# Optimization experiments

Hardware: AMD Instinct MI355X
Metric: run time of the kernel (lower is better)

The kernel has to match this reference:

```python
import jax, jax.numpy as jnp
import numpy as np

THRESH = 1e-5   # replace_denormals threshold
EPS = 1e-5      # instance_norm eps

NUM_LAYERS, TOKEN_LEN, EMBED = 24, 100, 1024
N, B = 1025, 8  # seq (incl. cls token), batch


def _replace_denormals(x):
    return jnp.where((x < THRESH) & (x > -THRESH), THRESH, x)


def _delta_feat(feats, tokens, w_t2f, b_t2f, w_df, b_df, instance_norm):
    # feats: [n, b, c], tokens: [m, c]
    attn = jnp.einsum('nbc,mc->nbm', feats, tokens)
    if instance_norm:  # normalize over m per (n, b), biased variance (torch F.instance_norm)
        mu = attn.mean(axis=-1, keepdims=True)
        var = attn.var(axis=-1, keepdims=True)
        attn = (attn - mu) / jnp.sqrt(var + EPS)
    attn = jax.nn.softmax(attn * (feats.shape[-1] ** -0.5), axis=-1)
    v = tokens[1:] @ w_t2f.T + b_t2f                     # [m-1, c]
    df = jnp.einsum('nbm,mc->nbc', attn[:, :, 1:], v)    # drop first token column
    return (df + feats) @ w_df.T + b_df


def setup_inputs() -> dict:
    key = jax.random.key(0)
    ks = jax.random.split(key, 12)
    C = EMBED
    inp = {
        'feats': jax.random.normal(ks[0], (N, B, C), dtype=jnp.float32),
        'learnable_tokens': jax.random.normal(ks[1], (NUM_LAYERS, TOKEN_LEN, C), dtype=jnp.float32) * 0.04,
        'learnable_tokens2': jax.random.normal(ks[2], (NUM_LAYERS, TOKEN_LEN, C), dtype=jnp.float32) * 0.04,
        'w_t2f': jax.random.normal(ks[3], (C, C), dtype=jnp.float32) * 0.02,
        'b_t2f': jax.random.normal(ks[4], (C,), dtype=jnp.float32) * 0.02,
        'w_df': jax.random.normal(ks[5], (C, C), dtype=jnp.float32) * 0.02,
        'b_df': jax.random.normal(ks[6], (C,), dtype=jnp.float32) * 0.02,
        'w_t2f2': jax.random.normal(ks[7], (C, C), dtype=jnp.float32) * 0.02,
        'b_t2f2': jax.random.normal(ks[8], (C,), dtype=jnp.float32) * 0.02,
        'w_df2': jax.random.normal(ks[9], (C, C), dtype=jnp.float32) * 0.02,
        'b_df2': jax.random.normal(ks[10], (C,), dtype=jnp.float32) * 0.02,
        'scale': jnp.float32(0.001),
        'layer': 0,
    }
    return inp


def reference(feats, learnable_tokens, learnable_tokens2,
              w_t2f, b_t2f, w_df, b_df,
              w_t2f2, b_t2f2, w_df2, b_df2,
              scale, layer):
    # batch_first=False, has_cls_token=True (defaults)
    C = feats.shape[-1]
    cls_tok, x = feats[:1], feats[1:]            # [1,b,c], [n,b,c]
    n, b = x.shape[0], x.shape[1]

    # decompose: fft2 over last two dims (b, c), norm='backward'
    f = jnp.fft.fft2(x)
    re, im = jnp.real(f), jnp.imag(f)
    amp = jnp.sqrt(_replace_denormals(re * re + im * im))
    phase = jnp.arctan2(im, _replace_denormals(re))

    t1 = learnable_tokens[layer]
    t2 = learnable_tokens2[layer]
    d_phase = _delta_feat(phase, t1, w_t2f, b_t2f, w_df, b_df, instance_norm=False)
    d_amp = _delta_feat(amp, t2, w_t2f2, b_t2f2, w_df2, b_df2, instance_norm=True)

    # compose: stacked last dim has size 2, dim 2 has size C -> divide by sqrt(C*2)
    z = (jnp.cos(d_phase) * d_amp + 1j * (jnp.sin(d_phase) * d_amp)) / np.float32(np.sqrt(C * 2.0))
    z = z[..., : C // 2 + 1]                      # torch irfft2 trims last dim to s[-1]//2+1
    delta = jnp.fft.irfft2(z, s=(b, C), norm='ortho')

    out = x + delta * scale
    return jnp.concatenate([cls_tok, out], axis=0)
```

## Files before the change

kernel.cpp:

```cpp
#include <hip/hip_runtime.h>
#include <cstddef>


using bf16x8 = __attribute__((ext_vector_type(8))) short;
using f32x4  = __attribute__((ext_vector_type(4))) float;

__device__ inline short f2bf(float f) {
  union { float f; unsigned u; } v; v.f = f;
  unsigned r = v.u + 0x7FFFu + ((v.u >> 16) & 1u);
  return (short)(r >> 16);
}
__device__ inline float bf2f(short s) {
  union { unsigned u; float f; } v; v.u = ((unsigned)(unsigned short)s) << 16;
  return v.f;
}
__device__ inline void async16(const void* g, void* l) {
  __builtin_amdgcn_global_load_lds(
      (const __attribute__((address_space(1))) void*)g,
      (__attribute__((address_space(3))) void*)l, 16, 0, 0);
}
__device__ inline float fast_atan2(float y, float x) {
  float ax = fabsf(x), ay = fabsf(y);
  float mx = fmaxf(ax, ay), mn = fminf(ax, ay);
  float a = mn * __frcp_rn(mx);
  float s = a * a;
  float r = fmaf(fmaf(fmaf(-0.0464964749f, s, 0.15931422f), s, -0.327622764f),
                 s * a, a);
  if (ay > ax) r = 1.5707963267948966f - r;
  if (x < 0.f) r = 3.14159265358979f - r;
  return (y < 0.f) ? -r : r;
}

__device__ inline int PADi(int i) { return i + (i >> 5); }
__device__ inline int rev4_8(int t) {
  return ((t & 3) << 6) | (((t >> 2) & 3) << 4) | (((t >> 4) & 3) << 2) | ((t >> 6) & 3);
}

__device__ inline void fft8_fwd(float* xr, float* xi) {
  const float r = 0.70710678118654752f;
  float ar[4], ai[4], br[4], bi[4], tr, ti;
  ar[0]=xr[0]+xr[4]; ai[0]=xi[0]+xi[4]; br[0]=xr[0]-xr[4]; bi[0]=xi[0]-xi[4];
  ar[1]=xr[1]+xr[5]; ai[1]=xi[1]+xi[5];
  tr=xr[1]-xr[5]; ti=xi[1]-xi[5]; br[1]=(tr+ti)*r; bi[1]=(ti-tr)*r;
  ar[2]=xr[2]+xr[6]; ai[2]=xi[2]+xi[6];
  tr=xr[2]-xr[6]; ti=xi[2]-xi[6]; br[2]=ti; bi[2]=-tr;
  ar[3]=xr[3]+xr[7]; ai[3]=xi[3]+xi[7];
  tr=xr[3]-xr[7]; ti=xi[3]-xi[7]; br[3]=(ti-tr)*r; bi[3]=-(tr+ti)*r;
  float u0r=ar[0]+ar[2], u0i=ai[0]+ai[2], u1r=ar[1]+ar[3], u1i=ai[1]+ai[3];
  float v0r=ar[0]-ar[2], v0i=ai[0]-ai[2];
  tr=ar[1]-ar[3]; ti=ai[1]-ai[3];
  float v1r=ti, v1i=-tr;
  xr[0]=u0r+u1r; xi[0]=u0i+u1i; xr[4]=u0r-u1r; xi[4]=u0i-u1i;
  xr[2]=v0r+v1r; xi[2]=v0i+v1i; xr[6]=v0r-v1r; xi[6]=v0i-v1i;
  u0r=br[0]+br[2]; u0i=bi[0]+bi[2]; u1r=br[1]+br[3]; u1i=bi[1]+bi[3];
  v0r=br[0]-br[2]; v0i=bi[0]-bi[2];
  tr=br[1]-br[3]; ti=bi[1]-bi[3];
  v1r=ti; v1i=-tr;
  xr[1]=u0r+u1r; xi[1]=u0i+u1i; xr[5]=u0r-u1r; xi[5]=u0i-u1i;
  xr[3]=v0r+v1r; xi[3]=v0i+v1i; xr[7]=v0r-v1r; xi[7]=v0i-v1i;
}
__device__ inline void fft8_inv(float* xr, float* xi) {
  const float r = 0.70710678118654752f;
  float ar[4], ai[4], br[4], bi[4], tr, ti;
  ar[0]=xr[0]+xr[4]; ai[0]=xi[0]+xi[4]; br[0]=xr[0]-xr[4]; bi[0]=xi[0]-xi[4];
  ar[1]=xr[1]+xr[5]; ai[1]=xi[1]+xi[5];
  tr=xr[1]-xr[5]; ti=xi[1]-xi[5]; br[1]=(tr-ti)*r; bi[1]=(tr+ti)*r;
  ar[2]=xr[2]+xr[6]; ai[2]=xi[2]+xi[6];
  tr=xr[2]-xr[6]; ti=xi[2]-xi[6]; br[2]=-ti; bi[2]=tr;
  ar[3]=xr[3]+xr[7]; ai[3]=xi[3]+xi[7];
  tr=xr[3]-xr[7]; ti=xi[3]-xi[7]; br[3]=-(tr+ti)*r; bi[3]=(tr-ti)*r;
  float u0r=ar[0]+ar[2], u0i=ai[0]+ai[2], u1r=ar[1]+ar[3], u1i=ai[1]+ai[3];
  float v0r=ar[0]-ar[2], v0i=ai[0]-ai[2];
  tr=ar[1]-ar[3]; ti=ai[1]-ai[3];
  float v1r=-ti, v1i=tr;
  xr[0]=u0r+u1r; xi[0]=u0i+u1i; xr[4]=u0r-u1r; xi[4]=u0i-u1i;
  xr[2]=v0r+v1r; xi[2]=v0i+v1i; xr[6]=v0r-v1r; xi[6]=v0i-v1i;
  u0r=br[0]+br[2]; u0i=bi[0]+bi[2]; u1r=br[1]+br[3]; u1i=bi[1]+bi[3];
  v0r=br[0]-br[2]; v0i=bi[0]-bi[2];
  tr=br[1]-br[3]; ti=bi[1]-bi[3];
  v1r=-ti; v1i=tr;
  xr[1]=u0r+u1r; xi[1]=u0i+u1i; xr[5]=u0r-u1r; xi[5]=u0i-u1i;
  xr[3]=v0r+v1r; xi[3]=v0i+v1i; xr[7]=v0r-v1r; xi[7]=v0i-v1i;
}

template <int SIGN, int NP>
__device__ inline void fft1024xN(float2 (*zb)[1056], int t) {
#pragma unroll
  for (int s = 0; s < 5; ++s) {
    const int Q = 256 >> (2 * s);
    const int j = t & (Q - 1);
    const int i0 = ((t & ~(Q - 1)) << 2) + j;
    const float ang = (float)SIGN * 6.283185307179586f * (float)j / (float)(4 * Q);
    float s1, c1; __sincosf(ang, &s1, &c1);
    const float c2 = c1 * c1 - s1 * s1, s2 = 2.f * c1 * s1;
    const float c3 = c2 * c1 - s2 * s1, s3 = c2 * s1 + s2 * c1;
#pragma unroll
    for (int p = 0; p < NP; ++p) {
      float2* z = zb[p];
      float2 x0 = z[PADi(i0)];
      float2 x1 = z[PADi(i0 + Q)];
      float2 x2 = z[PADi(i0 + 2 * Q)];
      float2 x3 = z[PADi(i0 + 3 * Q)];
      float t0x = x0.x + x2.x, t0y = x0.y + x2.y;
      float t1x = x0.x - x2.x, t1y = x0.y - x2.y;
      float t2x = x1.x + x3.x, t2y = x1.y + x3.y;
      float t3x = x1.x - x3.x, t3y = x1.y - x3.y;
      float u0x = t0x + t2x, u0y = t0y + t2y;
      float u2x = t0x - t2x, u2y = t0y - t2y;
      float u1x, u1y, u3x, u3y;
      if (SIGN < 0) { u1x = t1x + t3y; u1y = t1y - t3x; u3x = t1x - t3y; u3y = t1y + t3x; }
      else          { u1x = t1x - t3y; u1y = t1y + t3x; u3x = t1x + t3y; u3y = t1y - t3x; }
      z[PADi(i0)]         = make_float2(u0x, u0y);
      z[PADi(i0 + Q)]     = make_float2(u1x * c1 - u1y * s1, u1x * s1 + u1y * c1);
      z[PADi(i0 + 2 * Q)] = make_float2(u2x * c2 - u2y * s2, u2x * s2 + u2y * c2);
      z[PADi(i0 + 3 * Q)] = make_float2(u3x * c3 - u3y * s3, u3x * s3 + u3y * c3);
    }
    __syncthreads();
  }
}

__global__ __launch_bounds__(256) void fwd_fft2_amp_conv(
    const float* __restrict__ feats,
    short* __restrict__ ampb, short* __restrict__ phaseb,
    const float* __restrict__ w1, const float* __restrict__ w2,
    const float* __restrict__ w3, const float* __restrict__ w4,
    const float* __restrict__ lt1, const float* __restrict__ lt2,
    const int* __restrict__ layerp,
    short* __restrict__ Wdst, short* __restrict__ Tdst,
    float* __restrict__ out) {
  if (blockIdx.x >= 1024) {
    const int id = blockIdx.x - 1024;
    const int t4 = threadIdx.x * 4;
    if (id < 4096) {
      const int z = id >> 10, row = id & 1023;
      const float* W = (z == 0 ? w1 : z == 1 ? w2 : z == 2 ? w3 : w4)
                       + (size_t)row * 1024;
      short* D = Wdst + ((size_t)z * 1024 + row) * 1024;
      float4 v = *(const float4*)(W + t4);
      D[t4] = f2bf(v.x); D[t4 + 1] = f2bf(v.y); D[t4 + 2] = f2bf(v.z); D[t4 + 3] = f2bf(v.w);
    } else if (id < 4608) {
      const int i2 = id - 4096;
      const int zz = i2 >> 7, row = i2 & 127;
      const int z = zz & 1, shift = zz >> 1;
      short* D = Tdst + ((size_t)zz * 128 + row) * 1024;
      if (row + shift < 100) {
        const float* S = (z ? lt2 : lt1) + (size_t)layerp[0] * 102400
                         + (size_t)(row + shift) * 1024;
        float4 v = *(const float4*)(S + t4);
        D[t4] = f2bf(v.x); D[t4 + 1] = f2bf(v.y); D[t4 + 2] = f2bf(v.z); D[t4 + 3] = f2bf(v.w);
      } else {
        D[t4] = 0; D[t4 + 1] = 0; D[t4 + 2] = 0; D[t4 + 3] = 0;
      }
    } else {
      const int i = (id - 4608) * 256 + threadIdx.x;
      out[i] = feats[i];
    }
    return;
  }
  __shared__ float2 zb[4][1056];
  const int t = threadIdx.x;
  const int n = blockIdx.x;
  const float* base = feats + 8192 + (size_t)n * 8192;
#pragma unroll
  for (int p = 0; p < 4; ++p) {
    const float* x0 = base + (size_t)(2 * p) * 1024;
    const float* x1 = x0 + 1024;
#pragma unroll
    for (int m = 0; m < 4; ++m) {
      const int c = t + 256 * m;
      zb[p][PADi(c)] = make_float2(x0[c], x1[c]);
    }
  }
  __syncthreads();
  fft1024xN<-1, 4>(zb, t);
  const int rt = rev4_8(t);
  short* ab = ampb + (size_t)n * 8192;
  short* pb = phaseb + (size_t)n * 8192;
#pragma unroll
  for (int m = 0; m < 4; ++m) {
    const int k = 256 * m + t;
    const int kk = (1024 - k) & 1023;
    const int pos  = 4 * rt + m;
    const int pos2 = 4 * rev4_8(kk & 255) + (kk >> 8);
    float xr[8], xi[8];
#pragma unroll
    for (int p = 0; p < 4; ++p) {
      float2 Z = zb[p][PADi(pos)];
      float2 W = zb[p][PADi(pos2)];
      xr[2 * p]     = 0.5f * (Z.x + W.x);
      xi[2 * p]     = 0.5f * (Z.y - W.y);
      xr[2 * p + 1] = 0.5f * (Z.y + W.y);
      xi[2 * p + 1] = 0.5f * (W.x - Z.x);
    }
    fft8_fwd(xr, xi);
#pragma unroll
    for (int kb = 0; kb < 8; ++kb) {
      float sr = xr[kb], si = xi[kb];
      float r2 = sr * sr + si * si;
      if (r2 < 1e-5f) r2 = 1e-5f;
      float a = sqrtf(r2);
      float rr = (sr < 1e-5f && sr > -1e-5f) ? 1e-5f : sr;
      float ph = fast_atan2(si, rr);
      ab[kb * 1024 + k] = f2bf(a);
      pb[kb * 1024 + k] = f2bf(ph);
    }
  }
}

__global__ __launch_bounds__(256) void gemm_sm_v(
    const short* A0, const short* A1,
    const short* Tok,
    const short* Wall,
    const float* bt1, const float* bt2,
    short* __restrict__ awb,
    short* __restrict__ vrow) {
  __shared__ __align__(16) char smem[39040];
  const int z = blockIdx.z;
  const int tid = threadIdx.x;
  const int wave = tid >> 6, lane = tid & 63;
  const int m16 = lane & 15, quad = lane >> 4;
  const int fcol = ((quad ^ ((m16 >> 1) & 3)) * 8) + m16 * 32;
  const int r0 = tid >> 2;
  const int csw = (((tid & 3) ^ ((r0 >> 1) & 3)) * 8);

  if (blockIdx.x >= 256) {
    const int jb = blockIdx.x - 256;
    const short* A = Tok + (size_t)(2 + z) * 128 * 1024;
    const short* B = Wall + (size_t)z * 1024 * 1024;
    const float* bias = z ? bt2 : bt1;
    short* C = vrow + (size_t)z * 128 * 1024;
    const int K = 1024;
    short* As = (short*)smem;
    short* Bs = (short*)(smem + 8192);
    const int wm = (wave & 1) * 64, wn = (wave >> 1) * 64;
    f32x4 acc[4][4];
#pragma unroll
    for (int i = 0; i < 4; ++i)
#pragma unroll
      for (int j = 0; j < 4; ++j) acc[i][j] = (f32x4){0.f, 0.f, 0.f, 0.f};
    const short* aSrc0 = A + (size_t)r0 * K + csw;
    const short* aSrc1 = aSrc0 + (size_t)64 * K;
    const short* bSrc0 = B + (size_t)(jb * 128 + r0) * K + csw;
    const short* bSrc1 = bSrc0 + (size_t)64 * K;
    short* aDst0 = As + tid * 8;
    short* aDst1 = As + 2048 + tid * 8;
    short* bDst0 = Bs + tid * 8;
    short* bDst1 = Bs + 2048 + tid * 8;
    for (int k0 = 0; k0 < K; k0 += 32) {
      async16(aSrc0 + k0, aDst0);
      async16(aSrc1 + k0, aDst1);
      async16(bSrc0 + k0, bDst0);
      async16(bSrc1 + k0, bDst1);
      __syncthreads();
      bf16x8 af[4], bg[4];
#pragma unroll
      for (int ib = 0; ib < 4; ++ib)
        af[ib] = *(const bf16x8*)(As + (wm + ib * 16) * 32 + fcol);
#pragma unroll
      for (int jb2 = 0; jb2 < 4; ++jb2)
        bg[jb2] = *(const bf16x8*)(Bs + (wn + jb2 * 16) * 32 + fcol);
#pragma unroll
      for (int ib = 0; ib < 4; ++ib)
#pragma unroll
        for (int jb2 = 0; jb2 < 4; ++jb2)
          acc[ib][jb2] = __builtin_amdgcn_mfma_f32_16x16x32_bf16(af[ib], bg[jb2], acc[ib][jb2], 0, 0, 0);
      __syncthreads();
    }
#pragma unroll
    for (int ib = 0; ib < 4; ++ib) {
      const int rowb = wm + ib * 16 + quad * 4;
#pragma unroll
      for (int jb2 = 0; jb2 < 4; ++jb2) {
        const int col = jb * 128 + wn + jb2 * 16 + m16;
        const float bcv = bias[col];
#pragma unroll
        for (int r = 0; r < 4; ++r)
          C[(size_t)(rowb + r) * 1024 + col] = f2bf(acc[ib][jb2][r] + bcv);
      }
    }
    return;
  }

  const short* A = z ? A1 : A0;
  const short* B = Tok + (size_t)z * 128 * 1024;
  const int K = 1024;
  short* As = (short*)smem;
  short* Bs = (short*)(smem + 4096);
  float (*ltile)[129] = (float(*)[129])(smem + 20480);
  float (*red1)[8] = (float(*)[8])(smem + 36992);
  float (*red2)[8] = (float(*)[8])(smem + 38016);
  const int wm = (wave & 1) * 16, wn = (wave >> 1) * 64;
  f32x4 acc[4];
#pragma unroll
  for (int j = 0; j < 4; ++j) acc[j] = (f32x4){0.f, 0.f, 0.f, 0.f};
  const int asub = tid >> 7, aidx = tid & 127;
  const int ar0 = aidx >> 2;
  const int acsw = (((aidx & 3) ^ ((ar0 >> 1) & 3)) * 8);
  const short* aSrc = A + (size_t)(blockIdx.x * 32 + ar0) * K + acsw + asub * 32;
  short* aDst = As + asub * 1024 + aidx * 8;
  const short* bSrc0 = B + (size_t)r0 * K + csw;
  const short* bSrc1 = bSrc0 + (size_t)64 * K;
  short* bDst00 = Bs + tid * 8;
  short* bDst01 = Bs + 2048 + tid * 8;
  short* bDst10 = Bs + 4096 + tid * 8;
  short* bDst11 = Bs + 4096 + 2048 + tid * 8;
  for (int k0 = 0; k0 < K; k0 += 64) {
    async16(aSrc + k0, aDst);
    async16(bSrc0 + k0, bDst00);
    async16(bSrc1 + k0, bDst01);
    async16(bSrc0 + k0 + 32, bDst10);
    async16(bSrc1 + k0 + 32, bDst11);
    __syncthreads();
#pragma unroll
    for (int sub = 0; sub < 2; ++sub) {
      bf16x8 af = *(const bf16x8*)(As + sub * 1024 + wm * 32 + fcol);
      bf16x8 bg[4];
#pragma unroll
      for (int jb = 0; jb < 4; ++jb)
        bg[jb] = *(const bf16x8*)(Bs + sub * 4096 + (wn + jb * 16) * 32 + fcol);
#pragma unroll
      for (int jb = 0; jb < 4; ++jb)
        acc[jb] = __builtin_amdgcn_mfma_f32_16x16x32_bf16(af, bg[jb], acc[jb], 0, 0, 0);
    }
    __syncthreads();
  }
#pragma unroll
  for (int jb = 0; jb < 4; ++jb)
#pragma unroll
    for (int r = 0; r < 4; ++r)
      ltile[wm + quad * 4 + r][wn + jb * 16 + m16] = acc[jb][r];
  __syncthreads();
  const int row = tid >> 3, l8 = tid & 7;
  float s = 0.f, q = 0.f;
  for (int c = l8; c < 100; c += 8) { float x = ltile[row][c]; s += x; q += x * x; }
  red1[row][l8] = s; red2[row][l8] = q;
  __syncthreads();
  float ssum = 0.f, qsum = 0.f;
#pragma unroll
  for (int i = 0; i < 8; ++i) { ssum += red1[row][i]; qsum += red2[row][i]; }
  __syncthreads();
  const float mu = ssum * 0.01f;
  const float rinv = rsqrtf(fmaxf(qsum * 0.01f - mu * mu, 0.f) + 1e-5f);
  float mx = -3.4e38f;
  for (int c = l8; c < 100; c += 8) {
    float x = ltile[row][c];
    if (z == 1) x = (x - mu) * rinv;
    x *= 0.03125f;
    ltile[row][c] = x;
    mx = fmaxf(mx, x);
  }
  red1[row][l8] = mx;
  __syncthreads();
#pragma unroll
  for (int i = 0; i < 8; ++i) mx = fmaxf(mx, red1[row][i]);
  __syncthreads();
  float es = 0.f;
  for (int c = l8; c < 100; c += 8) {
    float e = __expf(ltile[row][c] - mx);
    ltile[row][c] = e; es += e;
  }
  red1[row][l8] = es;
  __syncthreads();
  float tot = 0.f;
#pragma unroll
  for (int i = 0; i < 8; ++i) tot += red1[row][i];
  const float inv = 1.f / tot;
  short* Aout = awb + ((size_t)z * 8192 + (size_t)blockIdx.x * 32 + row) * 128;
  for (int c = l8; c < 100; c += 8)
    if (c >= 1) Aout[c - 1] = f2bf(ltile[row][c] * inv);
  for (int k = l8; k < 128; k += 8)
    if (k >= 99) Aout[k] = 0;
}

__global__ __launch_bounds__(256) void gemm64(
    const short* A0, const short* A1,
    const short* B0, const short* B1,
    void* C0v, void* C1v, int K, int ldc) {
  const int z = blockIdx.z;
  const short* A = z ? A1 : A0;
  const short* B = z ? B1 : B0;
  void* Cv = z ? C1v : C0v;
  __shared__ __align__(16) short As[64 * 32];
  __shared__ __align__(16) short Bs[128 * 32];
  const int tid = threadIdx.x;
  const int wave = tid >> 6, lane = tid & 63;
  const int m16 = lane & 15, quad = lane >> 4;
  const int wm = (wave & 1) * 32, wn = (wave >> 1) * 64;
  f32x4 acc[2][4];
#pragma unroll
  for (int i = 0; i < 2; ++i)
#pragma unroll
    for (int j = 0; j < 4; ++j) acc[i][j] = (f32x4){0.f, 0.f, 0.f, 0.f};
  const int r0 = tid >> 2;
  const int csw = (((tid & 3) ^ ((r0 >> 1) & 3)) * 8);
  const short* aSrc  = A + (size_t)(blockIdx.x * 64 + r0) * K + csw;
  const short* bSrc0 = B + (size_t)r0 * K + csw;
  const short* bSrc1 = bSrc0 + (size_t)64 * K;
  short* aDst  = As + tid * 8;
  short* bDst0 = Bs + tid * 8;
  short* bDst1 = Bs + 2048 + tid * 8;
  const int fcol = ((quad ^ ((m16 >> 1) & 3)) * 8) + m16 * 32;
  for (int k0 = 0; k0 < K; k0 += 32) {
    async16(aSrc + k0, aDst);
    async16(bSrc0 + k0, bDst0);
    async16(bSrc1 + k0, bDst1);
    __syncthreads();
    bf16x8 af[2], bg[4];
#pragma unroll
    for (int ib = 0; ib < 2; ++ib)
      af[ib] = *(const bf16x8*)(As + (wm + ib * 16) * 32 + fcol);
#pragma unroll
    for (int jb = 0; jb < 4; ++jb)
      bg[jb] = *(const bf16x8*)(Bs + (wn + jb * 16) * 32 + fcol);
#pragma unroll
    for (int ib = 0; ib < 2; ++ib)
#pragma unroll
      for (int jb = 0; jb < 4; ++jb)
        acc[ib][jb] = __builtin_amdgcn_mfma_f32_16x16x32_bf16(af[ib], bg[jb], acc[ib][jb], 0, 0, 0);
    __syncthreads();
  }
#pragma unroll
  for (int ib = 0; ib < 2; ++ib) {
    const int rowb = blockIdx.x * 64 + wm + ib * 16 + quad * 4;
#pragma unroll
    for (int jb = 0; jb < 4; ++jb) {
      const int col = wn + jb * 16 + m16;
#pragma unroll
      for (int r = 0; r < 4; ++r)
        ((short*)Cv)[(size_t)(rowb + r) * ldc + col] = f2bf(acc[ib][jb][r]);
    }
  }
}

__global__ __launch_bounds__(256) void gemm128_dual(
    const short* A1_0, const short* A1_1,
    const short* B1_0, const short* B1_1,
    const short* A2_0, const short* A2_1,
    const short* B2_0, const short* B2_1,
    const float* bias0, const float* bias1,
    short* C0, short* C1, int K1, int K2, int ldc) {
  const int z = blockIdx.z;
  const short* A1 = z ? A1_1 : A1_0;
  const short* B1 = z ? B1_1 : B1_0;
  const short* A2 = z ? A2_1 : A2_0;
  const short* B2 = z ? B2_1 : B2_0;
  const float* bias = z ? bias1 : bias0;
  short* C = z ? C1 : C0;
  __shared__ __align__(16) short As[2][128 * 32];
  __shared__ __align__(16) short Bs[2][128 * 32];
  const int tid = threadIdx.x;
  const int wave = tid >> 6, lane = tid & 63;
  const int m16 = lane & 15, quad = lane >> 4;
  const int wm = (wave & 1) * 64, wn = (wave >> 1) * 64;
  f32x4 acc[4][4];
#pragma unroll
  for (int i = 0; i < 4; ++i)
#pragma unroll
    for (int j = 0; j < 4; ++j) acc[i][j] = (f32x4){0.f, 0.f, 0.f, 0.f};
  const int r0 = tid >> 2;
  const int csw = (((tid & 3) ^ ((r0 >> 1) & 3)) * 8);
  const int fcol = ((quad ^ ((m16 >> 1) & 3)) * 8) + m16 * 32;
#pragma unroll 1
  for (int phase = 0; phase < 2; ++phase) {
    const short* A = phase ? A2 : A1;
    const short* B = phase ? B2 : B1;
    const int K = phase ? K2 : K1;
    const short* aSrc0 = A + (size_t)(blockIdx.x * 128 + r0) * K + csw;
    const short* aSrc1 = aSrc0 + (size_t)64 * K;
    const short* bSrc0 = B + (size_t)(blockIdx.y * 128 + r0) * K + csw;
    const short* bSrc1 = bSrc0 + (size_t)64 * K;
    for (int k0 = 0; k0 < K; k0 += 64) {
      async16(aSrc0 + k0,      As[0] + tid * 8);
      async16(aSrc1 + k0,      As[0] + 2048 + tid * 8);
      async16(aSrc0 + k0 + 32, As[1] + tid * 8);
      async16(aSrc1 + k0 + 32, As[1] + 2048 + tid * 8);
      async16(bSrc0 + k0,      Bs[0] + tid * 8);
      async16(bSrc1 + k0,      Bs[0] + 2048 + tid * 8);
      async16(bSrc0 + k0 + 32, Bs[1] + tid * 8);
      async16(bSrc1 + k0 + 32, Bs[1] + 2048 + tid * 8);
      __syncthreads();
#pragma unroll
      for (int sub = 0; sub < 2; ++sub) {
        bf16x8 af[4], bg[4];
#pragma unroll
        for (int ib = 0; ib < 4; ++ib)
          af[ib] = *(const bf16x8*)(As[sub] + (wm + ib * 16) * 32 + fcol);
#pragma unroll
        for (int jb = 0; jb < 4; ++jb)
          bg[jb] = *(const bf16x8*)(Bs[sub] + (wn + jb * 16) * 32 + fcol);
#pragma unroll
        for (int ib = 0; ib < 4; ++ib)
#pragma unroll
          for (int jb = 0; jb < 4; ++jb)
            acc[ib][jb] = __builtin_amdgcn_mfma_f32_16x16x32_bf16(af[ib], bg[jb], acc[ib][jb], 0, 0, 0);
      }
      __syncthreads();
    }
  }
#pragma unroll
  for (int ib = 0; ib < 4; ++ib) {
    const int rowb = blockIdx.x * 128 + wm + ib * 16 + quad * 4;
#pragma unroll
    for (int jb = 0; jb < 4; ++jb) {
      const int col = blockIdx.y * 128 + wn + jb * 16 + m16;
      const float bcv = bias[col];
#pragma unroll
      for (int r = 0; r < 4; ++r) {
        const size_t idx = (size_t)(rowb + r) * (size_t)ldc + col;
        C[idx] = f2bf(acc[ib][jb][r] + bcv);
      }
    }
  }
}

__global__ __launch_bounds__(256) void inv_fft2_res(const short* __restrict__ dPb,
                                                    const short* __restrict__ dAb,
                                                    const float* __restrict__ feats,
                                                    const float* __restrict__ scalep,
                                                    float* __restrict__ out) {
  __shared__ float2 zb[2][1056];
  const int t = threadIdx.x;
  const int n = blockIdx.x >> 1, q = blockIdx.x & 1;
  const short* pp = dPb + (size_t)n * 8192;
  const short* ap = dAb + (size_t)n * 8192;
  const float invs = 0.022097086912079608f;
  const float inv8 = 0.35355339059327373f;
  for (int k = t; k < 513; k += 256) {
    float zr[8], zi[8];
#pragma unroll
    for (int b = 0; b < 8; ++b) {
      float p = bf2f(pp[b * 1024 + k]);
      float a = bf2f(ap[b * 1024 + k]) * invs;
      float s, c; __sincosf(p, &s, &c);
      zr[b] = c * a; zi[b] = s * a;
    }
    fft8_inv(zr, zi);
#pragma unroll
    for (int l = 0; l < 2; ++l) {
      const int bp = 4 * q + 2 * l;
      float ax = zr[bp] * inv8,     ay = zi[bp] * inv8;
      float bx = zr[bp + 1] * inv8, by = zi[bp + 1] * inv8;
      zb[l][PADi(k)] = make_float2(ax - by, ay + bx);
      if (k >= 1 && k <= 511)
        zb[l][PADi(1024 - k)] = make_float2(ax + by, bx - ay);
    }
  }
  __syncthreads();
  fft1024xN<1, 2>(zb, t);
  const int rt = rev4_8(t);
  const float s = scalep[0] * 0.03125f;
#pragma unroll
  for (int l = 0; l < 2; ++l) {
    const int p4 = 2 * q + l;
    const size_t ob0 = 8192 + ((size_t)n * 8 + 2 * p4) * 1024;
    const size_t ob1 = ob0 + 1024;
#pragma unroll
    for (int m = 0; m < 4; ++m) {
      const int nn = 256 * m + t;
      float2 y = zb[l][PADi(4 * rt + m)];
      out[ob0 + nn] = feats[ob0 + nn] + y.x * s;
      out[ob1 + nn] = feats[ob1 + nn] + y.y * s;
    }
  }
}

extern "C" void kernel_launch(void* const* d_in, const int* in_sizes, int n_in,
                              void* d_out, int out_size, void* d_ws, size_t ws_size,
                              hipStream_t stream) {
  const float* feats  = (const float*)d_in[0];
  const float* lt1    = (const float*)d_in[1];
  const float* lt2    = (const float*)d_in[2];
  const float* w_t2f  = (const float*)d_in[3];
  const float* b_t2f  = (const float*)d_in[4];
  const float* w_df   = (const float*)d_in[5];
  const float* b_df   = (const float*)d_in[6];
  const float* w_t2f2 = (const float*)d_in[7];
  const float* b_t2f2 = (const float*)d_in[8];
  const float* w_df2  = (const float*)d_in[9];
  const float* b_df2  = (const float*)d_in[10];
  const float* scalep = (const float*)d_in[11];
  const int*   layerp = (const int*)d_in[12];
  float* out = (float*)d_out;
  (void)in_sizes; (void)n_in; (void)out_size; (void)ws_size;

  const size_t SZ = 8192ull * 1024ull;
  short* Pa   = (short*)d_ws;
  short* Pb   = Pa + SZ;
  short* awb  = Pb + SZ;
  short* Tok  = awb + 2ull * 8192 * 128;
  short* Wall = Tok + 4ull * 128 * 1024;
  short* vrow = Wall + 4ull * 1024 * 1024;
  short* V2T  = vrow + 2ull * 128 * 1024;
  short* dP   = V2T + 2ull * 1024 * 128;
  short* dA   = dP + SZ;

  fwd_fft2_amp_conv<<<dim3(5664), dim3(256), 0, stream>>>(
      feats, Pb, Pa, w_t2f, w_t2f2, w_df, w_df2, lt1, lt2, layerp,
      Wall, Tok, out);
  gemm_sm_v<<<dim3(264, 1, 2), dim3(256), 0, stream>>>(
      Pa, Pb, Tok, Wall, b_t2f, b_t2f2, awb, vrow);
  gemm64<<<dim3(16, 1, 2), dim3(256), 0, stream>>>(
      Wall + 2 * 1024 * 1024, Wall + 3 * 1024 * 1024,
      vrow, vrow + 128 * 1024,
      V2T, V2T + 1024 * 128, 1024, 128);
  gemm128_dual<<<dim3(64, 8, 2), dim3(256), 0, stream>>>(
      awb, awb + 8192 * 128, V2T, V2T + 1024 * 128,
      Pa, Pb, Wall + 2 * 1024 * 1024, Wall + 3 * 1024 * 1024,
      b_df, b_df2, dP, dA, 128, 1024, 1024);
  inv_fft2_res<<<dim3(2048), dim3(256), 0, stream>>>(dP, dA, feats, scalep, out);
}
```

Before: 254.8 us.

## Rewrite dual GEMM as 256x256 tile with 4-stage async LDS pipeline

Replaces the 128x128 dual-phase GEMM with a 256x256 tile kernel using 512 threads, each wave computing 128x64. Both K phases are merged into one linear loop over 32-wide K slices, prefetched three stages ahead into a 4-buffer LDS ring, with counted vmcnt waits instead of full barriers around each load. MFMA sections are bracketed by s_setprio to favour matrix issue. The aim is more data reuse per tile and hiding global-load latency. In exchange it uses far more LDS and registers and launches only 256 blocks, which may underfill the GPU.

```diff
diff --git a/kernel.cpp b/kernel.cpp
--- a/kernel.cpp
+++ b/kernel.cpp
@@ -432,7 +432,63 @@
   }
 }
 
-__global__ __launch_bounds__(256) void gemm128_dual(
+#define DUAL_STEP(VM, DOISS)                                                 \
+  do {                                                                       \
+    asm volatile("s_waitcnt vmcnt(" #VM ")" ::: "memory");                   \
+    __builtin_amdgcn_s_barrier();                                            \
+    __builtin_amdgcn_sched_barrier(0);                                       \
+    if (DOISS) {                                                             \
+      const int kp = k + 3;                                                  \
+      short* ad = &As[kp & 3][0];                                            \
+      short* bd = &Bs[kp & 3][0];                                            \
+      const short *as0, *as1, *bs0, *bs1;                                    \
+      if (kp < NS1) {                                                        \
+        const int c = kp << 5;                                               \
+        as0 = A1 + aO1_0 + c; as1 = A1 + aO1_1 + c;                          \
+        bs0 = B1 + bO1_0 + c; bs1 = B1 + bO1_1 + c;                          \
+      } else {                                                               \
+        const int c = (kp - NS1) << 5;                                       \
+        as0 = A2 + aO2_0 + c; as1 = A2 + aO2_1 + c;                          \
+        bs0 = B2 + bO2_0 + c; bs1 = B2 + bO2_1 + c;                          \
+      }                                                                      \
+      async16(as0, ad + tid * 8);                                            \
+      async16(as1, ad + 4096 + tid * 8);                                     \
+      async16(bs0, bd + tid * 8);                                            \
+      async16(bs1, bd + 4096 + tid * 8);                                     \
+    }                                                                        \
+    {                                                                        \
+      const short* Asl = &As[k & 3][0];                                      \
+      const short* Bsl = &Bs[k & 3][0];                                      \
+      bf16x8 bg[4], af[4];                                                   \
+      _Pragma("unroll")                                                      \
+      for (int jb = 0; jb < 4; ++jb)                                         \
+        bg[jb] = *(const bf16x8*)(Bsl + (wn + jb * 16) * 32 + fcol);         \
+      _Pragma("unroll")                                                      \
+      for (int ib = 0; ib < 4; ++ib)                                         \
+        af[ib] = *(const bf16x8*)(Asl + (wm + ib * 16) * 32 + fcol);         \
+      __builtin_amdgcn_s_setprio(1);                                         \
+      _Pragma("unroll")                                                      \
+      for (int ib = 0; ib < 4; ++ib)                                         \
+        _Pragma("unroll")                                                    \
+        for (int jb = 0; jb < 4; ++jb)                                       \
+          acc[ib][jb] = __builtin_amdgcn_mfma_f32_16x16x32_bf16(             \
+              af[ib], bg[jb], acc[ib][jb], 0, 0, 0);                         \
+      __builtin_amdgcn_s_setprio(0);                                         \
+      _Pragma("unroll")                                                      \
+      for (int ib = 0; ib < 4; ++ib)                                         \
+        af[ib] = *(const bf16x8*)(Asl + (wm + 64 + ib * 16) * 32 + fcol);    \
+      __builtin_amdgcn_s_setprio(1);                                         \
+      _Pragma("unroll")                                                      \
+      for (int ib = 0; ib < 4; ++ib)                                         \
+        _Pragma("unroll")                                                    \
+        for (int jb = 0; jb < 4; ++jb)                                       \
+          acc[ib + 4][jb] = __builtin_amdgcn_mfma_f32_16x16x32_bf16(         \
+              af[ib], bg[jb], acc[ib + 4][jb], 0, 0, 0);                     \
+      __builtin_amdgcn_s_setprio(0);                                         \
+    }                                                                        \
+  } while (0)
+
+__global__ __launch_bounds__(512) void gemm256_dual(
     const short* A1_0, const short* A1_1,
     const short* B1_0, const short* B1_1,
     const short* A2_0, const short* A2_1,
@@ -446,63 +502,61 @@
   const short* B2 = z ? B2_1 : B2_0;
   const float* bias = z ? bias1 : bias0;
   short* C = z ? C1 : C0;
-  __shared__ __align__(16) short As[2][128 * 32];
-  __shared__ __align__(16) short Bs[2][128 * 32];
+  __shared__ __align__(16) short As[4][8192];
+  __shared__ __align__(16) short Bs[4][8192];
   const int tid = threadIdx.x;
   const int wave = tid >> 6, lane = tid & 63;
   const int m16 = lane & 15, quad = lane >> 4;
-  const int wm = (wave & 1) * 64, wn = (wave >> 1) * 64;
-  f32x4 acc[4][4];
-#pragma unroll
-  for (int i = 0; i < 4; ++i)
-#pragma unroll
-    for (int j = 0; j < 4; ++j) acc[i][j] = (f32x4){0.f, 0.f, 0.f, 0.f};
+  const int wm = (wave & 1) * 128, wn = (wave >> 1) * 64;
+  const int fcol = ((quad ^ ((m16 >> 1) & 3)) * 8) + m16 * 32;
   const int r0 = tid >> 2;
   const int csw = (((tid & 3) ^ ((r0 >> 1) & 3)) * 8);
-  const int fcol = ((quad ^ ((m16 >> 1) & 3)) * 8) + m16 * 32;
+  const size_t aO1_0 = (size_t)(blockIdx.x * 256 + r0) * (size_t)K1 + csw;
+  const size_t aO1_1 = aO1_0 + (size_t)128 * K1;
+  const size_t bO1_0 = (size_t)(blockIdx.y * 256 + r0) * (size_t)K1 + csw;
+  const size_t bO1_1 = bO1_0 + (size_t)128 * K1;
+  const size_t aO2_0 = (size_t)(blockIdx.x * 256 + r0) * (size_t)K2 + csw;
+  const size_t aO2_1 = aO2_0 + (size_t)128 * K2;
+  const size_t bO2_0 = (size_t)(blockIdx.y * 256 + r0) * (size_t)K2 + csw;
+  const size_t bO2_1 = bO2_0 + (size_t)128 * K2;
+  const int NS1 = K1 >> 5;
+  const int NT  = NS1 + (K2 >> 5);
+  f32x4 acc[8][4];
+#pragma unroll
+  for (int i = 0; i < 8; ++i)
+#pragma unroll
+    for (int j = 0; j < 4; ++j) acc[i][j] = (f32x4){0.f, 0.f, 0.f, 0.f};
+#pragma unroll
+  for (int k = 0; k < 3; ++k) {
+    short* ad = &As[k & 3][0];
+    short* bd = &Bs[k & 3][0];
+    const short *as0, *as1, *bs0, *bs1;
+    if (k < NS1) {
+      const int c = k << 5;
+      as0 = A1 + aO1_0 + c; as1 = A1 + aO1_1 + c;
+      bs0 = B1 + bO1_0 + c; bs1 = B1 + bO1_1 + c;
+    } else {
+      const int c = (k - NS1) << 5;
+      as0 = A2 + aO2_0 + c; as1 = A2 + aO2_1 + c;
+      bs0 = B2 + bO2_0 + c; bs1 = B2 + bO2_1 + c;
+    }
+    async16(as0, ad + tid * 8);
+    async16(as1, ad + 4096 + tid * 8);
+    async16(bs0, bd + tid * 8);
+    async16(bs1, bd + 4096 + tid * 8);
+  }
 #pragma unroll 1
-  for (int phase = 0; phase < 2; ++phase) {
-    const short* A = phase ? A2 : A1;
-    const short* B = phase ? B2 : B1;
-    const int K = phase ? K2 : K1;
-    const short* aSrc0 = A + (size_t)(blockIdx.x * 128 + r0) * K + csw;
-    const short* aSrc1 = aSrc0 + (size_t)64 * K;
-    const short* bSrc0 = B + (size_t)(blockIdx.y * 128 + r0) * K + csw;
-    const short* bSrc1 = bSrc0 + (size_t)64 * K;
-    for (int k0 = 0; k0 < K; k0 += 64) {
-      async16(aSrc0 + k0,      As[0] + tid * 8);
-      async16(aSrc1 + k0,      As[0] + 2048 + tid * 8);
-      async16(aSrc0 + k0 + 32, As[1] + tid * 8);
-      async16(aSrc1 + k0 + 32, As[1] + 2048 + tid * 8);
-      async16(bSrc0 + k0,      Bs[0] + tid * 8);
-      async16(bSrc1 + k0,      Bs[0] + 2048 + tid * 8);
-      async16(bSrc0 + k0 + 32, Bs[1] + tid * 8);
-      async16(bSrc1 + k0 + 32, Bs[1] + 2048 + tid * 8);
-      __syncthreads();
-#pragma unroll
-      for (int sub = 0; sub < 2; ++sub) {
-        bf16x8 af[4], bg[4];
-#pragma unroll
-        for (int ib = 0; ib < 4; ++ib)
-          af[ib] = *(const bf16x8*)(As[sub] + (wm + ib * 16) * 32 + fcol);
-#pragma unroll
-        for (int jb = 0; jb < 4; ++jb)
-          bg[jb] = *(const bf16x8*)(Bs[sub] + (wn + jb * 16) * 32 + fcol);
-#pragma unroll
-        for (int ib = 0; ib < 4; ++ib)
-#pragma unroll
-          for (int jb = 0; jb < 4; ++jb)
-            acc[ib][jb] = __builtin_amdgcn_mfma_f32_16x16x32_bf16(af[ib], bg[jb], acc[ib][jb], 0, 0, 0);
-      }
-      __syncthreads();
-    }
-  }
-#pragma unroll
-  for (int ib = 0; ib < 4; ++ib) {
-    const int rowb = blockIdx.x * 128 + wm + ib * 16 + quad * 4;
+  for (int k = 0; k < NT - 2; ++k) {
+    DUAL_STEP(8, (k + 3 < NT));
+  }
+  { const int k = NT - 2; DUAL_STEP(4, false); }
+  { const int k = NT - 1; DUAL_STEP(0, false); }
+#pragma unroll
+  for (int ib = 0; ib < 8; ++ib) {
+    const int rowb = blockIdx.x * 256 + wm + ib * 16 + quad * 4;
 #pragma unroll
     for (int jb = 0; jb < 4; ++jb) {
-      const int col = blockIdx.y * 128 + wn + jb * 16 + m16;
+      const int col = blockIdx.y * 256 + wn + jb * 16 + m16;
       const float bcv = bias[col];
 #pragma unroll
       for (int r = 0; r < 4; ++r) {
@@ -512,6 +566,7 @@
     }
   }
 }
+#undef DUAL_STEP
 
 __global__ __launch_bounds__(256) void inv_fft2_res(const short* __restrict__ dPb,
                                                     const short* __restrict__ dAb,
@@ -603,7 +658,7 @@
       Wall + 2 * 1024 * 1024, Wall + 3 * 1024 * 1024,
       vrow, vrow + 128 * 1024,
       V2T, V2T + 1024 * 128, 1024, 128);
-  gemm128_dual<<<dim3(64, 8, 2), dim3(256), 0, stream>>>(
+  gemm256_dual<<<dim3(32, 4, 2), dim3(512), 0, stream>>>(
       awb, awb + 8192 * 128, V2T, V2T + 1024 * 128,
       Pa, Pb, Wall + 2 * 1024 * 1024, Wall + 3 * 1024 * 1024,
       b_df, b_df2, dP, dA, 128, 1024, 1024);
```

After: 255.9 us. About the same (+0.4%).
